# Optimization experiments

Hardware: AMD Instinct MI355X
Metric: run time of the kernel (lower is better)

## Reference

```python
import jax, jax.numpy as jnp
import numpy as np
import math

SEQ_LEN = 2048
DIM = 4096
N_HEADS = 32
N_KV_HEADS = 8
HEAD_DIM = DIM // N_HEADS  # 128
ROPE_THETA = 500000.0
W_SCALE = 0.02


def _precompute_freqs(head_dim, end, theta=ROPE_THETA):
    freq = 1.0 / theta ** (jnp.arange(0, head_dim, 2, dtype=jnp.float32) / head_dim)  # [hd/2]
    t = jnp.arange(end, dtype=jnp.float32)
    f = t[:, None] * freq[None, :]  # [S, hd/2]
    return jnp.cos(f), jnp.sin(f)


def _apply_rope(x, cos, sin):
    # x: [S, H, hd]; interleaved even/odd rotation, matching torch ::2 / 1::2 indexing
    xe = x[:, :, 0::2]
    xo = x[:, :, 1::2]
    c = cos[:, None, :]  # [S, 1, hd/2]
    s = sin[:, None, :]
    re = xe * c - xo * s
    ro = xe * s + xo * c
    # re-interleave: out[..., 2i] = re[..., i], out[..., 2i+1] = ro[..., i]
    return jnp.stack([re, ro], axis=-1).reshape(x.shape)


def setup_inputs() -> dict:
    key = jax.random.key(0)
    k = jax.random.split(key, 5)
    x = jax.random.normal(k[0], (SEQ_LEN, DIM), dtype=jnp.float32)
    wq = jax.random.normal(k[1], (DIM, DIM), dtype=jnp.float32) * W_SCALE
    wk = jax.random.normal(k[2], (N_KV_HEADS * HEAD_DIM, DIM), dtype=jnp.float32) * W_SCALE
    wv = jax.random.normal(k[3], (N_KV_HEADS * HEAD_DIM, DIM), dtype=jnp.float32) * W_SCALE
    wo = jax.random.normal(k[4], (DIM, DIM), dtype=jnp.float32) * W_SCALE
    return {"x": x, "wq": wq, "wk": wk, "wv": wv, "wo": wo}


def reference(x, wq, wk, wv, wo):
    S = SEQ_LEN
    rep = N_HEADS // N_KV_HEADS  # 4

    Q = (x @ wq.T).reshape(S, N_HEADS, HEAD_DIM)
    K = (x @ wk.T).reshape(S, N_KV_HEADS, HEAD_DIM)
    V = (x @ wv.T).reshape(S, N_KV_HEADS, HEAD_DIM)

    cos, sin = _precompute_freqs(HEAD_DIM, S)
    Q = _apply_rope(Q, cos, sin)
    K = _apply_rope(K, cos, sin)

    # GQA: repeat_interleave(K, rep, dim=1) maps query head h -> kv group h // rep.
    # Express natively with a grouped einsum instead of materializing repeated K/V.
    Qg = Q.transpose(1, 0, 2).reshape(N_KV_HEADS, rep, S, HEAD_DIM)  # [g, r, S, d]
    Kt = K.transpose(1, 0, 2)  # [g, S, d]
    Vt = V.transpose(1, 0, 2)  # [g, S, d]

    scores = jnp.einsum('grqd,gkd->grqk', Qg, Kt) / math.sqrt(HEAD_DIM)
    mask = jnp.triu(jnp.full((S, S), -jnp.inf, dtype=scores.dtype), k=1)
    probs = jax.nn.softmax(scores + mask, axis=-1)
    out = jnp.einsum('grqk,gkd->grqd', probs, Vt)  # [g, r, S, d]

    out = out.reshape(N_HEADS, S, HEAD_DIM).transpose(1, 0, 2).reshape(S, N_HEADS * HEAD_DIM)
    return out @ wo.T
```

## Files before the change

kernel.cpp:

```cpp
#include <hip/hip_runtime.h>

typedef unsigned short u16;
typedef short short8 __attribute__((ext_vector_type(8)));
typedef float f32x4 __attribute__((ext_vector_type(4)));
typedef unsigned short u16x4 __attribute__((ext_vector_type(4)));

typedef short8 short8_a __attribute__((may_alias));
typedef f32x4 f32x4_a __attribute__((may_alias));
typedef u16x4 u16x4_a __attribute__((may_alias));
typedef unsigned int uint_a __attribute__((may_alias));

__device__ __forceinline__ u16 f2b(float f) {
  unsigned u = __float_as_uint(f);
  u += 0x7FFFu + ((u >> 16) & 1u);
  return (u16)(u >> 16);
}

__device__ __forceinline__ void mfma_b(f32x4& d, short8 a, short8 b) {
  asm("v_mfma_f32_16x16x32_bf16 %0, %1, %2, %0" : "+v"(d) : "v"(a), "v"(b));
}

__device__ __forceinline__ void guard4(f32x4& a, f32x4& b, f32x4& c, f32x4& d) {
  asm volatile("s_nop 7\n\ts_nop 7" : "+v"(a), "+v"(b), "+v"(c), "+v"(d));
}
__device__ __forceinline__ void guard8(f32x4* o) {
  asm volatile("s_nop 7\n\ts_nop 7"
               : "+v"(o[0]), "+v"(o[1]), "+v"(o[2]), "+v"(o[3]),
                 "+v"(o[4]), "+v"(o[5]), "+v"(o[6]), "+v"(o[7]));
}

__device__ __forceinline__ void gload16(const void* g, void* l) {
  __builtin_amdgcn_global_load_lds((__attribute__((address_space(1))) void*)(g),
                                   (__attribute__((address_space(3))) void*)(l),
                                   16, 0, 0);
}

__device__ __forceinline__ void bar_v0() {
  asm volatile("s_waitcnt vmcnt(0)\n\ts_barrier" ::: "memory");
}
__device__ __forceinline__ void bar_v3() {
  asm volatile("s_waitcnt vmcnt(3)\n\ts_barrier" ::: "memory");
}

__global__ __launch_bounds__(256)
void k_prep(const float* __restrict__ x, const float* __restrict__ wq,
            const float* __restrict__ wk, const float* __restrict__ wv,
            u16* __restrict__ xb, u16* __restrict__ wB,
            float* __restrict__ cost, float* __restrict__ sint) {
  const long i = (long)blockIdx.x * 256 + threadIdx.x;
  const float* src;
  u16* dst;
  long j;
  if (i < 6291456) {
    if (i < 2097152) { src = x; dst = xb; j = i; }
    else { src = wq; dst = wB; j = i - 2097152; }
  } else if (i < 8388608) {
    if (i < 7340032) { src = wk; dst = wB + 16777216; j = i - 6291456; }
    else { src = wv; dst = wB + 20971520; j = i - 7340032; }
  } else {
    long ti = i - 8388608;
    int s = (int)(ti >> 6), jj = (int)(ti & 63);
    float freq = powf(500000.0f, -(float)jj * (1.0f / 64.0f));
    float a = (float)s * freq;
    float sv, cv;
    sincosf(a, &sv, &cv);
    cost[ti] = cv;
    sint[ti] = sv;
    return;
  }
  f32x4 v = ((const f32x4_a*)src)[j];
  u16x4 o;
  o[0] = f2b(v[0]); o[1] = f2b(v[1]); o[2] = f2b(v[2]); o[3] = f2b(v[3]);
  ((u16x4_a*)dst)[j] = o;
}

#define QK_SCALE 0.08838834764831845f
__global__ __launch_bounds__(512, 2)
void k_gemmQ(const u16* __restrict__ A, const u16* __restrict__ B,
             const float* __restrict__ cost, const float* __restrict__ sint,
             u16* __restrict__ Qb, u16* __restrict__ Kb, u16* __restrict__ Vt) {
  extern __shared__ u16 ldsq[];
  u16* As = ldsq;
  u16* Bs = ldsq + 12288;
  const int K = 4096;
  const int tid = threadIdx.x;
  const int w = tid >> 6, lane = tid & 63;
  const int hi = lane >> 4, lo = lane & 15;
  const int wr = w >> 2, wc = w & 3;
  int bid = blockIdx.x;
  bid = (bid & 7) * 48 + (bid >> 3);
  const int tm = bid / 24, tn = bid - (bid / 24) * 24;
  const int m0 = tm << 7, n0 = tn << 8;

  const int r2 = tid >> 2;
  const int ks = (((tid & 3) ^ ((tid >> 3) & 3)) << 3);
  const u16* Ag = A + (long)(m0 + r2) * K + ks;
  const u16* Bg0 = B + (long)(n0 + r2) * K + ks;
  const u16* Bg1 = B + (long)(n0 + 128 + r2) * K + ks;
  const int sb = w * 512;

  f32x4 acc[4][4] = {};
  const int hs = hi ^ ((lo >> 1) & 3);
  const int aoff = (wr * 64 + lo) * 32 + hs * 8;
  const int boff = (wc * 64 + lo) * 32 + hs * 8;

  const int nt = K >> 5;
  int i0 = 0, i1 = 1, i2 = 2;

#define STGQ(kt, bi)                                      \
  {                                                       \
    gload16(Ag + (kt)*32, As + (bi)*4096 + sb);           \
    gload16(Bg0 + (kt)*32, Bs + (bi)*8192 + sb);          \
    gload16(Bg1 + (kt)*32, Bs + (bi)*8192 + 4096 + sb);   \
  }

  STGQ(0, 0);
  STGQ(1, 1);
  bar_v3();

  for (int t = 0; t < nt; ++t) {
    if (t + 2 < nt) STGQ(t + 2, i2);
    short8 af[4], bf[4];
#pragma unroll
    for (int m = 0; m < 4; ++m)
      af[m] = *(const short8_a*)(As + i0 * 4096 + aoff + m * 512);
#pragma unroll
    for (int n = 0; n < 4; ++n)
      bf[n] = *(const short8_a*)(Bs + i0 * 8192 + boff + n * 512);
    __builtin_amdgcn_s_setprio(1);
#pragma unroll
    for (int m = 0; m < 4; ++m)
#pragma unroll
      for (int n = 0; n < 4; ++n) mfma_b(acc[m][n], af[m], bf[n]);
    __builtin_amdgcn_s_setprio(0);
    if (t + 2 < nt) bar_v3();
    else bar_v0();
    const int tmp = i0; i0 = i1; i1 = i2; i2 = tmp;
  }
#undef STGQ
  guard8(&acc[0][0]);
  guard8(&acc[2][0]);

  if (n0 < 5120) {
    const bool isQ = (n0 < 4096);
#pragma unroll
    for (int m = 0; m < 4; ++m) {
      const int row0 = m0 + wr * 64 + m * 16 + hi * 4;
#pragma unroll
      for (int n = 0; n < 4; ++n) {
        const int c = n0 + wc * 64 + n * 16 + lo;
        const int j0 = (c & 127) >> 1;
        const bool even = ((c & 1) == 0);
#pragma unroll
        for (int r = 0; r < 4; ++r) {
          float own = acc[m][n][r];
          float part = __shfl_xor(own, 1);
          const int s_ = row0 + r;
          const float cv = cost[s_ * 64 + j0];
          const float sv = sint[s_ * 64 + j0];
          float res = even ? (own * cv - part * sv) : (part * sv + own * cv);
          if (isQ)
            Qb[(long)s_ * 4096 + c] = f2b(res * QK_SCALE);
          else
            Kb[(long)s_ * 1024 + (c - 4096)] = f2b(res);
        }
      }
    }
  } else {
#pragma unroll
    for (int m = 0; m < 4; ++m) {
      const int row0 = m0 + wr * 64 + m * 16 + hi * 4;
#pragma unroll
      for (int n = 0; n < 4; ++n) {
        const int vc = n0 - 5120 + wc * 64 + n * 16 + lo;
        u16x4 pk;
#pragma unroll
        for (int r = 0; r < 4; ++r) pk[r] = f2b(acc[m][n][r]);
        *(u16x4_a*)(Vt + (long)vc * 2048 + row0) = pk;
      }
    }
  }
}

__global__ __launch_bounds__(512, 2)
void k_gemm_t2(const u16* __restrict__ A, const u16* __restrict__ B,
               float* __restrict__ C) {
  extern __shared__ u16 lds2[];
  u16* As = lds2;
  u16* Bs = lds2 + 12288;
  const int K = 4096, N = 4096;
  const int tid = threadIdx.x;
  const int w = tid >> 6, lane = tid & 63;
  const int hi = lane >> 4, lo = lane & 15;
  const int wr = w >> 2, wc = w & 3;
  int bid = blockIdx.x;
  bid = (bid & 7) * 32 + (bid >> 3);
  const int tm = bid >> 4, tn = bid & 15;
  const int m0 = tm << 7, n0 = tn << 8;

  const int r2 = tid >> 2;
  const int ks = (((tid & 3) ^ ((tid >> 3) & 3)) << 3);
  const u16* Ag = A + (long)(m0 + r2) * K + ks;
  const u16* Bg0 = B + (long)(n0 + r2) * K + ks;
  const u16* Bg1 = B + (long)(n0 + 128 + r2) * K + ks;
  const int sb = w * 512;

  f32x4 acc[4][4] = {};
  const int hs = hi ^ ((lo >> 1) & 3);
  const int aoff = (wr * 64 + lo) * 32 + hs * 8;
  const int boff = (wc * 64 + lo) * 32 + hs * 8;

  const int nt = K >> 5;
  int i0 = 0, i1 = 1, i2 = 2;

#define STG2(kt, bi)                                      \
  {                                                       \
    gload16(Ag + (kt)*32, As + (bi)*4096 + sb);           \
    gload16(Bg0 + (kt)*32, Bs + (bi)*8192 + sb);          \
    gload16(Bg1 + (kt)*32, Bs + (bi)*8192 + 4096 + sb);   \
  }

  STG2(0, 0);
  STG2(1, 1);
  bar_v3();

  for (int t = 0; t < nt; ++t) {
    if (t + 2 < nt) STG2(t + 2, i2);
    short8 af[4], bf[4];
#pragma unroll
    for (int m = 0; m < 4; ++m)
      af[m] = *(const short8_a*)(As + i0 * 4096 + aoff + m * 512);
#pragma unroll
    for (int n = 0; n < 4; ++n)
      bf[n] = *(const short8_a*)(Bs + i0 * 8192 + boff + n * 512);
    __builtin_amdgcn_s_setprio(1);
#pragma unroll
    for (int m = 0; m < 4; ++m)
#pragma unroll
      for (int n = 0; n < 4; ++n) mfma_b(acc[m][n], af[m], bf[n]);
    __builtin_amdgcn_s_setprio(0);
    if (t + 2 < nt) bar_v3();
    else bar_v0();
    const int tmp = i0; i0 = i1; i1 = i2; i2 = tmp;
  }
#undef STG2
  guard8(&acc[0][0]);
  guard8(&acc[2][0]);

#pragma unroll
  for (int m = 0; m < 4; ++m) {
    const int row0 = m0 + wr * 64 + m * 16 + hi * 4;
#pragma unroll
    for (int n = 0; n < 4; ++n) {
      const int col = n0 + wc * 64 + n * 16 + lo;
#pragma unroll
      for (int r = 0; r < 4; ++r)
        C[(long)(row0 + r) * N + col] = acc[m][n][r];
    }
  }
}

#define KLD 136
#define VLD 72
__global__ __launch_bounds__(256, 2)
void k_attn(const u16* __restrict__ Qb, const u16* __restrict__ Kb,
            const u16* __restrict__ Vt, u16* __restrict__ Ab,
            const float* __restrict__ wo, u16* __restrict__ wob) {
  {
    const long base = (long)blockIdx.x * 256 + threadIdx.x;
#pragma unroll
    for (int c = 0; c < 16; ++c) {
      const long idx = base + (long)c * 262144;
      f32x4 v = ((const f32x4_a*)wo)[idx];
      u16x4 o;
      o[0] = f2b(v[0]); o[1] = f2b(v[1]); o[2] = f2b(v[2]); o[3] = f2b(v[3]);
      ((u16x4_a*)wob)[idx] = o;
    }
  }

  __shared__ u16 Ks[64 * KLD];
  __shared__ u16 Vs[128 * VLD];
  __shared__ u16 Ps[4 * 16 * VLD];

  const int tid = threadIdx.x;
  const int w = tid >> 6, lane = tid & 63;
  const int hi = lane >> 4, lo = lane & 15;
  const int qt = 31 - (blockIdx.x >> 5);
  const int h = blockIdx.x & 31;
  const int hkv = h >> 2;
  const int q0 = qt * 64;
  const int qrow = q0 + w * 16 + lo;

  short8 qf[4];
#pragma unroll
  for (int c = 0; c < 4; ++c)
    qf[c] = *(const short8_a*)(Qb + (long)qrow * 4096 + h * 128 + c * 32 + hi * 8);

  f32x4 o[8] = {};
  float m_run = -1e30f, l_run = 0.f;
  u16* Pw = Ps + w * (16 * VLD);

  const int ntiles = qt + 1;
  for (int t = 0; t < ntiles; ++t) {
    const int kv0 = t * 64;
    __syncthreads();
#pragma unroll
    for (int r = 0; r < 4; ++r) {
      int i = r * 256 + tid;
      int key = i >> 4, d8 = (i & 15) * 8;
      short8 v = *(const short8_a*)(Kb + (long)(kv0 + key) * 1024 + hkv * 128 + d8);
      *(short8_a*)(Ks + key * KLD + d8) = v;
    }
#pragma unroll
    for (int r = 0; r < 4; ++r) {
      int i = r * 256 + tid;
      int dd = i >> 3, k8 = (i & 7) * 8;
      short8 v = *(const short8_a*)(Vt + (long)hkv * 262144 + (long)dd * 2048 + kv0 + k8);
      *(short8_a*)(Vs + dd * VLD + k8) = v;
    }
    __syncthreads();

    f32x4 sc[4] = {};
#pragma unroll
    for (int c = 0; c < 4; ++c) {
#pragma unroll
      for (int kt = 0; kt < 4; ++kt) {
        short8 kf = *(const short8_a*)(Ks + (kt * 16 + lo) * KLD + c * 32 + hi * 8);
        mfma_b(sc[kt], kf, qf[c]);
      }
    }
    guard4(sc[0], sc[1], sc[2], sc[3]);

    if (t == ntiles - 1) {
#pragma unroll
      for (int kt = 0; kt < 4; ++kt)
#pragma unroll
        for (int r = 0; r < 4; ++r) {
          int key = kv0 + kt * 16 + hi * 4 + r;
          if (key > qrow) sc[kt][r] = -1e30f;
        }
    }
    float tmax = -1e30f;
#pragma unroll
    for (int kt = 0; kt < 4; ++kt)
#pragma unroll
      for (int r = 0; r < 4; ++r) tmax = fmaxf(tmax, sc[kt][r]);
    tmax = fmaxf(tmax, __shfl_xor(tmax, 16));
    tmax = fmaxf(tmax, __shfl_xor(tmax, 32));
    float m_new = fmaxf(m_run, tmax);
    float scale = __expf(m_run - m_new);
    float psum = 0.f;
    float p[16];
#pragma unroll
    for (int kt = 0; kt < 4; ++kt)
#pragma unroll
      for (int r = 0; r < 4; ++r) {
        float pv = __expf(sc[kt][r] - m_new);
        p[kt * 4 + r] = pv;
        psum += pv;
      }
    psum += __shfl_xor(psum, 16);
    psum += __shfl_xor(psum, 32);
    l_run = l_run * scale + psum;
    m_run = m_new;
    float srow[4];
#pragma unroll
    for (int r = 0; r < 4; ++r) srow[r] = __shfl(scale, hi * 4 + r);
#pragma unroll
    for (int n = 0; n < 8; ++n)
#pragma unroll
      for (int r = 0; r < 4; ++r) o[n][r] *= srow[r];
#pragma unroll
    for (int kt = 0; kt < 4; ++kt) {
      unsigned p01 = (unsigned)f2b(p[kt * 4]) | ((unsigned)f2b(p[kt * 4 + 1]) << 16);
      unsigned p23 = (unsigned)f2b(p[kt * 4 + 2]) | ((unsigned)f2b(p[kt * 4 + 3]) << 16);
      *(uint_a*)(Pw + lo * VLD + kt * 16 + hi * 4) = p01;
      *(uint_a*)(Pw + lo * VLD + kt * 16 + hi * 4 + 2) = p23;
    }
    __syncthreads();
#pragma unroll
    for (int c = 0; c < 2; ++c) {
      short8 pf = *(const short8_a*)(Pw + lo * VLD + c * 32 + hi * 8);
#pragma unroll
      for (int n = 0; n < 8; ++n) {
        short8 vf = *(const short8_a*)(Vs + (n * 16 + lo) * VLD + c * 32 + hi * 8);
        mfma_b(o[n], pf, vf);
      }
    }
  }
  guard8(o);

  float inv = 1.0f / l_run;
  float irow[4];
#pragma unroll
  for (int r = 0; r < 4; ++r) irow[r] = __shfl(inv, hi * 4 + r);
#pragma unroll
  for (int n = 0; n < 8; ++n)
#pragma unroll
    for (int r = 0; r < 4; ++r) {
      int q = q0 + w * 16 + hi * 4 + r;
      Ab[(long)q * 4096 + h * 128 + n * 16 + lo] = f2b(o[n][r] * irow[r]);
    }
}

extern "C" void kernel_launch(void* const* d_in, const int* in_sizes, int n_in,
                              void* d_out, int out_size, void* d_ws, size_t ws_size,
                              hipStream_t stream) {
  const float* x = (const float*)d_in[0];
  const float* wq = (const float*)d_in[1];
  const float* wk = (const float*)d_in[2];
  const float* wv = (const float*)d_in[3];
  const float* wo = (const float*)d_in[4];
  float* out = (float*)d_out;
  char* ws = (char*)d_ws;

  size_t off = 0;
  u16* xb = (u16*)(ws + off); off += 16777216;
  u16* wB = (u16*)(ws + off); off += 50331648;
  u16* wob = (u16*)(ws + off); off += 33554432;
  u16* Qb = (u16*)(ws + off); off += 16777216;
  u16* Kb = (u16*)(ws + off); off += 4194304;
  u16* Vtb = (u16*)(ws + off); off += 4194304;
  float* cost = (float*)(ws + off); off += 524288;
  float* sint = (float*)(ws + off); off += 524288;
  u16* Ab = (u16*)(ws + off); off += 16777216;

  static bool attr_set = false;
  if (!attr_set) {
    hipFuncSetAttribute((const void*)k_gemmQ,
                        hipFuncAttributeMaxDynamicSharedMemorySize, 73728);
    hipFuncSetAttribute((const void*)k_gemm_t2,
                        hipFuncAttributeMaxDynamicSharedMemorySize, 73728);
    attr_set = true;
  }

  k_prep<<<33280, 256, 0, stream>>>(x, wq, wk, wv, xb, wB, cost, sint);

  k_gemmQ<<<384, 512, 73728, stream>>>(xb, wB, cost, sint, Qb, Kb, Vtb);

  k_attn<<<1024, 256, 0, stream>>>(Qb, Kb, Vtb, Ab, wo, wob);

  k_gemm_t2<<<256, 512, 73728, stream>>>(Ab, wob, out);
}
```

Baseline: 372.4 us.

## Transpose QKV GEMM operands, move wo conversion to prep, add MFMA priority

The QKV projection GEMM now takes weights as the M operand and activations as the N operand. Each lane therefore holds even/odd RoPE pairs in its own accumulator registers, which removes the cross-lane shuffle and lets Q/K be written as packed 4-element stores, while V^T stores become per-element. The wo fp32-to-bf16 conversion moves out of the attention kernel into the prep kernel, so prep launches more blocks and attention no longer carries that prologue. s_setprio is added around the MFMA sections in attention to favour matrix issue.

```diff
diff --git a/kernel.cpp b/kernel.cpp
--- a/kernel.cpp
+++ b/kernel.cpp
@@ -45,28 +45,32 @@
 __global__ __launch_bounds__(256)
 void k_prep(const float* __restrict__ x, const float* __restrict__ wq,
             const float* __restrict__ wk, const float* __restrict__ wv,
-            u16* __restrict__ xb, u16* __restrict__ wB,
+            const float* __restrict__ wo, u16* __restrict__ xb,
+            u16* __restrict__ wB, u16* __restrict__ wob,
             float* __restrict__ cost, float* __restrict__ sint) {
   const long i = (long)blockIdx.x * 256 + threadIdx.x;
-  const float* src;
-  u16* dst;
-  long j;
-  if (i < 6291456) {
-    if (i < 2097152) { src = x; dst = xb; j = i; }
-    else { src = wq; dst = wB; j = i - 2097152; }
-  } else if (i < 8388608) {
-    if (i < 7340032) { src = wk; dst = wB + 16777216; j = i - 6291456; }
-    else { src = wv; dst = wB + 20971520; j = i - 7340032; }
-  } else {
-    long ti = i - 8388608;
-    int s = (int)(ti >> 6), jj = (int)(ti & 63);
+  if (i < 131072) {
+    int s = (int)(i >> 6), jj = (int)(i & 63);
     float freq = powf(500000.0f, -(float)jj * (1.0f / 64.0f));
     float a = (float)s * freq;
     float sv, cv;
     sincosf(a, &sv, &cv);
-    cost[ti] = cv;
-    sint[ti] = sv;
+    cost[i] = cv;
+    sint[i] = sv;
     return;
+  }
+  const long q = i - 131072;
+  const float* src;
+  u16* dst;
+  long j;
+  if (q < 6291456) {
+    if (q < 2097152) { src = x; dst = xb; j = q; }
+    else { src = wq; dst = wB; j = q - 2097152; }
+  } else if (q < 8388608) {
+    if (q < 7340032) { src = wk; dst = wB + 16777216; j = q - 6291456; }
+    else { src = wv; dst = wB + 20971520; j = q - 7340032; }
+  } else {
+    src = wo; dst = wob; j = q - 8388608;
   }
   f32x4 v = ((const f32x4_a*)src)[j];
   u16x4 o;
@@ -76,12 +80,12 @@
 
 #define QK_SCALE 0.08838834764831845f
 __global__ __launch_bounds__(512, 2)
-void k_gemmQ(const u16* __restrict__ A, const u16* __restrict__ B,
+void k_gemmT(const u16* __restrict__ Wb, const u16* __restrict__ Xb,
              const float* __restrict__ cost, const float* __restrict__ sint,
              u16* __restrict__ Qb, u16* __restrict__ Kb, u16* __restrict__ Vt) {
-  extern __shared__ u16 ldsq[];
-  u16* As = ldsq;
-  u16* Bs = ldsq + 12288;
+  extern __shared__ u16 ldsT[];
+  u16* As = ldsT;
+  u16* Bs = ldsT + 12288;
   const int K = 4096;
   const int tid = threadIdx.x;
   const int w = tid >> 6, lane = tid & 63;
@@ -89,14 +93,15 @@
   const int wr = w >> 2, wc = w & 3;
   int bid = blockIdx.x;
   bid = (bid & 7) * 48 + (bid >> 3);
-  const int tm = bid / 24, tn = bid - (bid / 24) * 24;
-  const int m0 = tm << 7, n0 = tn << 8;
+  const int tm = bid >> 3, tn = bid & 7;
+  const int m0 = tm << 7;
+  const int n0 = tn << 8;
 
   const int r2 = tid >> 2;
   const int ks = (((tid & 3) ^ ((tid >> 3) & 3)) << 3);
-  const u16* Ag = A + (long)(m0 + r2) * K + ks;
-  const u16* Bg0 = B + (long)(n0 + r2) * K + ks;
-  const u16* Bg1 = B + (long)(n0 + 128 + r2) * K + ks;
+  const u16* Ag = Wb + (long)(m0 + r2) * K + ks;
+  const u16* Bg0 = Xb + (long)(n0 + r2) * K + ks;
+  const u16* Bg1 = Xb + (long)(n0 + 128 + r2) * K + ks;
   const int sb = w * 512;
 
   f32x4 acc[4][4] = {};
@@ -107,19 +112,19 @@
   const int nt = K >> 5;
   int i0 = 0, i1 = 1, i2 = 2;
 
-#define STGQ(kt, bi)                                      \
+#define STGT(kt, bi)                                      \
   {                                                       \
     gload16(Ag + (kt)*32, As + (bi)*4096 + sb);           \
     gload16(Bg0 + (kt)*32, Bs + (bi)*8192 + sb);          \
     gload16(Bg1 + (kt)*32, Bs + (bi)*8192 + 4096 + sb);   \
   }
 
-  STGQ(0, 0);
-  STGQ(1, 1);
+  STGT(0, 0);
+  STGT(1, 1);
   bar_v3();
 
   for (int t = 0; t < nt; ++t) {
-    if (t + 2 < nt) STGQ(t + 2, i2);
+    if (t + 2 < nt) STGT(t + 2, i2);
     short8 af[4], bf[4];
 #pragma unroll
     for (int m = 0; m < 4; ++m)
@@ -137,46 +142,49 @@
     else bar_v0();
     const int tmp = i0; i0 = i1; i1 = i2; i2 = tmp;
   }
-#undef STGQ
+#undef STGT
   guard8(&acc[0][0]);
   guard8(&acc[2][0]);
 
-  if (n0 < 5120) {
-    const bool isQ = (n0 < 4096);
+  if (m0 < 5120) {
+    const bool isQ = (m0 < 4096);
 #pragma unroll
     for (int m = 0; m < 4; ++m) {
-      const int row0 = m0 + wr * 64 + m * 16 + hi * 4;
+      const int nb = m0 + wr * 64 + m * 16 + hi * 4;
+      const int j0 = (nb & 127) >> 1;
 #pragma unroll
       for (int n = 0; n < 4; ++n) {
-        const int c = n0 + wc * 64 + n * 16 + lo;
-        const int j0 = (c & 127) >> 1;
-        const bool even = ((c & 1) == 0);
-#pragma unroll
-        for (int r = 0; r < 4; ++r) {
-          float own = acc[m][n][r];
-          float part = __shfl_xor(own, 1);
-          const int s_ = row0 + r;
-          const float cv = cost[s_ * 64 + j0];
-          const float sv = sint[s_ * 64 + j0];
-          float res = even ? (own * cv - part * sv) : (part * sv + own * cv);
-          if (isQ)
-            Qb[(long)s_ * 4096 + c] = f2b(res * QK_SCALE);
-          else
-            Kb[(long)s_ * 1024 + (c - 4096)] = f2b(res);
+        const int s_ = n0 + wc * 64 + n * 16 + lo;
+        const float c0 = cost[s_ * 64 + j0], s0v = sint[s_ * 64 + j0];
+        const float c1 = cost[s_ * 64 + j0 + 1], s1v = sint[s_ * 64 + j0 + 1];
+        float e0 = acc[m][n][0], o0 = acc[m][n][1];
+        float e1 = acc[m][n][2], o1 = acc[m][n][3];
+        u16x4 pk;
+        if (isQ) {
+          pk[0] = f2b((e0 * c0 - o0 * s0v) * QK_SCALE);
+          pk[1] = f2b((e0 * s0v + o0 * c0) * QK_SCALE);
+          pk[2] = f2b((e1 * c1 - o1 * s1v) * QK_SCALE);
+          pk[3] = f2b((e1 * s1v + o1 * c1) * QK_SCALE);
+          *(u16x4_a*)(Qb + (long)s_ * 4096 + nb) = pk;
+        } else {
+          pk[0] = f2b(e0 * c0 - o0 * s0v);
+          pk[1] = f2b(e0 * s0v + o0 * c0);
+          pk[2] = f2b(e1 * c1 - o1 * s1v);
+          pk[3] = f2b(e1 * s1v + o1 * c1);
+          *(u16x4_a*)(Kb + (long)s_ * 1024 + (nb - 4096)) = pk;
         }
       }
     }
   } else {
 #pragma unroll
     for (int m = 0; m < 4; ++m) {
-      const int row0 = m0 + wr * 64 + m * 16 + hi * 4;
+      const int vc = m0 + wr * 64 + m * 16 + hi * 4 - 5120;
 #pragma unroll
       for (int n = 0; n < 4; ++n) {
-        const int vc = n0 - 5120 + wc * 64 + n * 16 + lo;
-        u16x4 pk;
-#pragma unroll
-        for (int r = 0; r < 4; ++r) pk[r] = f2b(acc[m][n][r]);
-        *(u16x4_a*)(Vt + (long)vc * 2048 + row0) = pk;
+        const int s_ = n0 + wc * 64 + n * 16 + lo;
+#pragma unroll
+        for (int r = 0; r < 4; ++r)
+          Vt[(long)(vc + r) * 2048 + s_] = f2b(acc[m][n][r]);
       }
     }
   }
@@ -264,20 +272,7 @@
 #define VLD 72
 __global__ __launch_bounds__(256, 2)
 void k_attn(const u16* __restrict__ Qb, const u16* __restrict__ Kb,
-            const u16* __restrict__ Vt, u16* __restrict__ Ab,
-            const float* __restrict__ wo, u16* __restrict__ wob) {
-  {
-    const long base = (long)blockIdx.x * 256 + threadIdx.x;
-#pragma unroll
-    for (int c = 0; c < 16; ++c) {
-      const long idx = base + (long)c * 262144;
-      f32x4 v = ((const f32x4_a*)wo)[idx];
-      u16x4 o;
-      o[0] = f2b(v[0]); o[1] = f2b(v[1]); o[2] = f2b(v[2]); o[3] = f2b(v[3]);
-      ((u16x4_a*)wob)[idx] = o;
-    }
-  }
-
+            const u16* __restrict__ Vt, u16* __restrict__ Ab) {
   __shared__ u16 Ks[64 * KLD];
   __shared__ u16 Vs[128 * VLD];
   __shared__ u16 Ps[4 * 16 * VLD];
@@ -321,6 +316,7 @@
     __syncthreads();
 
     f32x4 sc[4] = {};
+    __builtin_amdgcn_s_setprio(1);
 #pragma unroll
     for (int c = 0; c < 4; ++c) {
 #pragma unroll
@@ -329,6 +325,7 @@
         mfma_b(sc[kt], kf, qf[c]);
       }
     }
+    __builtin_amdgcn_s_setprio(0);
     guard4(sc[0], sc[1], sc[2], sc[3]);
 
     if (t == ntiles - 1) {
@@ -378,6 +375,7 @@
       *(uint_a*)(Pw + lo * VLD + kt * 16 + hi * 4 + 2) = p23;
     }
     __syncthreads();
+    __builtin_amdgcn_s_setprio(1);
 #pragma unroll
     for (int c = 0; c < 2; ++c) {
       short8 pf = *(const short8_a*)(Pw + lo * VLD + c * 32 + hi * 8);
@@ -387,6 +385,7 @@
         mfma_b(o[n], pf, vf);
       }
     }
+    __builtin_amdgcn_s_setprio(0);
   }
   guard8(o);
 
@@ -427,18 +426,18 @@
 
   static bool attr_set = false;
   if (!attr_set) {
-    hipFuncSetAttribute((const void*)k_gemmQ,
+    hipFuncSetAttribute((const void*)k_gemmT,
                         hipFuncAttributeMaxDynamicSharedMemorySize, 73728);
     hipFuncSetAttribute((const void*)k_gemm_t2,
                         hipFuncAttributeMaxDynamicSharedMemorySize, 73728);
     attr_set = true;
   }
 
-  k_prep<<<33280, 256, 0, stream>>>(x, wq, wk, wv, xb, wB, cost, sint);
-
-  k_gemmQ<<<384, 512, 73728, stream>>>(xb, wB, cost, sint, Qb, Kb, Vtb);
-
-  k_attn<<<1024, 256, 0, stream>>>(Qb, Kb, Vtb, Ab, wo, wob);
+  k_prep<<<49664, 256, 0, stream>>>(x, wq, wk, wv, wo, xb, wB, wob, cost, sint);
+
+  k_gemmT<<<384, 512, 73728, stream>>>(wB, xb, cost, sint, Qb, Kb, Vtb);
+
+  k_attn<<<1024, 256, 0, stream>>>(Qb, Kb, Vtb, Ab);
 
   k_gemm_t2<<<256, 512, 73728, stream>>>(Ab, wob, out);
 }
```

Measured after the change: 327.3 us. 1.14x faster.
